# Kernel optimization log

Measured on AMD Instinct MI355X. Metric: run time of the kernel, lower is better.

The kernel has to match this reference:

```python
import jax, jax.numpy as jnp
import numpy as np

NH, D, MULT, NLAYER = 8, 512, 32, 3
N_INT = D * MULT // NH  # 2048 sparse-code dim per head
EPS = 1e-5
THETA = 2.0 ** 16
NUM_CLASSES = 2


def _ln(x):
    # LayerNorm over last dim, no affine (elementwise_affine=False), biased var
    m = jnp.mean(x, axis=-1, keepdims=True)
    v = jnp.mean((x - m) ** 2, axis=-1, keepdims=True)
    return (x - m) * jax.lax.rsqrt(v + EPS)


def _rotate_half(x):
    x1, x2 = jnp.split(x, 2, axis=-1)
    return jnp.concatenate((-x2, x1), axis=-1)


def _attn(Qs, V):
    # Qs: [B,nh,T,N] ReLU-sparse codes (Q == K), V: [B,1,T,D] raw hidden
    T = Qs.shape[2]
    half = 1.0 / (THETA ** (jnp.arange(0, N_INT, 2, dtype=jnp.float32) / N_INT))
    freqs = jnp.concatenate((half, half))                      # [N]
    ph = jnp.arange(T, dtype=jnp.float32)[:, None] * freqs[None, :]  # [T,N]
    QR = Qs * jnp.cos(ph) + _rotate_half(Qs) * jnp.sin(ph)
    scores = jnp.einsum('bhtn,bhsn->bhts', QR, QR)             # no softmax, no scaling
    mask = jnp.tril(jnp.ones((T, T), dtype=scores.dtype), k=-1)  # strictly causal
    scores = scores * mask
    return jnp.einsum('bhts,bsd->bhtd', scores, V[:, 0])       # [B,nh,T,D]


def setup_inputs():
    key = jax.random.key(0)
    ks = jax.random.split(key, 8)
    B, T, NA, F = 2, 1024, 93, 4
    in_dim, out_dim = NA * F, NA * NUM_CLASSES
    s = 0.02
    return dict(
        x=jax.random.normal(ks[0], (B, T, NA, F), dtype=jnp.float32),
        Wi=jax.random.normal(ks[1], (in_dim, D), dtype=jnp.float32) * s,
        bi=jnp.zeros((D,), jnp.float32),
        enc=jax.random.uniform(ks[2], (NH, D, N_INT), jnp.float32, -s, s),
        enc_v=jax.random.uniform(ks[3], (NH, D, N_INT), jnp.float32, -s, s),
        dec=jax.random.uniform(ks[4], (NH * N_INT, D), jnp.float32, -s, s),
        Wo=jax.random.normal(ks[5], (D, out_dim), dtype=jnp.float32) * s,
        bo=jnp.zeros((out_dim,), jnp.float32),
    )


def reference(x, Wi, bi, enc, enc_v, dec, Wo, bo):
    B, T, NA, F = x.shape
    h = _ln((x.reshape(B, T, NA * F) @ Wi + bi)[:, None])      # [B,1,T,D]
    for _ in range(NLAYER):
        h_res = h
        h_sp = jax.nn.relu(jnp.einsum('bxtd,hdn->bhtn', h, enc))      # [B,nh,T,N]
        yKV = _ln(_attn(h_sp, h))                                     # [B,nh,T,D]
        y_sp = jax.nn.relu(jnp.einsum('bhtd,hdn->bhtn', yKV, enc_v))  # [B,nh,T,N]
        xy = h_sp * y_sp                                              # gating
        # transpose(1,2).reshape(B,1,T,nh*N): head-major flatten of codes
        xy_flat = xy.transpose(0, 2, 1, 3).reshape(B, 1, T, NH * N_INT)
        h = _ln(h_res + _ln(xy_flat @ dec))                           # [B,1,T,D]
    out = h[:, 0] @ Wo + bo                                           # [B,T,NA*C]
    return out.reshape(B, T, NA, NUM_CLASSES)
```

## Files before the change

### kernel.cpp

```cpp
#include <hip/hip_runtime.h>

typedef __bf16 bf16;
typedef __attribute__((ext_vector_type(8))) __bf16 bf16x8;
typedef __attribute__((ext_vector_type(4))) float f32x4;
typedef __attribute__((ext_vector_type(2))) _Float16 h16x2;

#define T_SEQ 1024
#define D_MODEL 512
#define N_INT 2048
#define NHEADS 8
#define IN_DIM 372
#define IN_PAD 384
#define OUT_DIM 186
#define OUT_PAD 256

__device__ inline void gld16(const bf16* g, bf16* l) {
  __builtin_amdgcn_global_load_lds((const __attribute__((address_space(1))) void*)g,
                                   (__attribute__((address_space(3))) void*)l, 16, 0, 0);
}

__device__ inline void block_sum2(float& a, float& b, float* red) {
#pragma unroll
  for (int o = 32; o > 0; o >>= 1) {
    a += __shfl_down(a, o, 64);
    b += __shfl_down(b, o, 64);
  }
  __syncthreads();
  if ((threadIdx.x & 63) == 0) {
    int w = threadIdx.x >> 6;
    red[2 * w] = a;
    red[2 * w + 1] = b;
  }
  __syncthreads();
  a = red[0] + red[2] + red[4] + red[6];
  b = red[1] + red[3] + red[5] + red[7];
}

__global__ __launch_bounds__(256) void transpose_cvt(const float* __restrict__ in,
                                                     bf16* __restrict__ out,
                                                     int rows, int cols) {
  __shared__ float tile[32][33];
  size_t zoff = (size_t)blockIdx.z * rows * cols;
  in += zoff;
  out += zoff;
  int c0 = blockIdx.x * 32, r0 = blockIdx.y * 32;
#pragma unroll
  for (int i = threadIdx.y; i < 32; i += 8)
    tile[i][threadIdx.x] = in[(size_t)(r0 + i) * cols + c0 + threadIdx.x];
  __syncthreads();
#pragma unroll
  for (int i = threadIdx.y; i < 32; i += 8)
    out[(size_t)(c0 + i) * rows + r0 + threadIdx.x] = (bf16)tile[threadIdx.x][i];
}

__global__ __launch_bounds__(256) void pad_trans(const float* __restrict__ in,
                                                 bf16* __restrict__ out,
                                                 int R, int C, int outLd) {
  __shared__ float tile[32][33];
  int c0 = blockIdx.x * 32, r0 = blockIdx.y * 32;
#pragma unroll
  for (int i = threadIdx.y; i < 32; i += 8) {
    int r = r0 + i, c = c0 + threadIdx.x;
    tile[i][threadIdx.x] = (r < R && c < C) ? in[(size_t)r * C + c] : 0.f;
  }
  __syncthreads();
#pragma unroll
  for (int i = threadIdx.y; i < 32; i += 8)
    out[(size_t)(c0 + i) * outLd + r0 + threadIdx.x] = (bf16)tile[threadIdx.x][i];
}

__global__ __launch_bounds__(256) void cvt_pad_x(const float* __restrict__ x,
                                                 bf16* __restrict__ xbf) {
  size_t r = blockIdx.x;
  for (int c = threadIdx.x; c < IN_PAD; c += 256)
    xbf[r * IN_PAD + c] = (c < IN_DIM) ? (bf16)x[r * IN_DIM + c] : (bf16)0.f;
}

__global__ __launch_bounds__(256) void rope_tables(h16x2* __restrict__ cs) {
  int t = blockIdx.x;
  for (int i = threadIdx.x; i < 1024; i += 256) {
    float ph = (float)t * exp2f(-16.0f * (float)i * (1.0f / 1024.0f));
    h16x2 v;
    v[0] = (_Float16)cosf(ph);
    v[1] = (_Float16)sinf(ph);
    cs[(size_t)t * 1024 + i] = v;
  }
}

__global__ __launch_bounds__(256) void ln0(const float* __restrict__ zin,
                                           float* __restrict__ h, bf16* __restrict__ hbf,
                                           bf16* __restrict__ hT) {
  __shared__ float red[8];
  size_t r = blockIdx.x;
  int tid = threadIdx.x;
  float v0 = zin[r * 512 + tid], v1 = zin[r * 512 + tid + 256];
  float s = v0 + v1, s2 = v0 * v0 + v1 * v1;
  block_sum2(s, s2, red);
  float mean = s * (1.f / 512.f);
  float var = s2 * (1.f / 512.f) - mean * mean;
  float rs = rsqrtf(var + 1e-5f);
  float o0 = (v0 - mean) * rs, o1 = (v1 - mean) * rs;
  h[r * 512 + tid] = o0;
  h[r * 512 + tid + 256] = o1;
  hbf[r * 512 + tid] = (bf16)o0;
  hbf[r * 512 + tid + 256] = (bf16)o1;
  int b = (int)(r >> 10), t = (int)(r & (T_SEQ - 1));
  hT[((size_t)b * 512 + tid) * T_SEQ + t] = (bf16)o0;
  hT[((size_t)b * 512 + tid + 256) * T_SEQ + t] = (bf16)o1;
}

__global__ __launch_bounds__(256) void ln_rows(bf16* __restrict__ io) {
  const int wid = threadIdx.x >> 6, lane = threadIdx.x & 63;
  size_t r = (size_t)blockIdx.x * 4 + wid;
  bf16* p = io + r * 512 + lane * 8;
  bf16x8 v = *(const bf16x8*)p;
  float f[8], s = 0.f, s2 = 0.f;
#pragma unroll
  for (int j = 0; j < 8; ++j) {
    f[j] = (float)v[j];
    s += f[j];
    s2 += f[j] * f[j];
  }
#pragma unroll
  for (int o = 32; o > 0; o >>= 1) {
    s += __shfl_xor(s, o, 64);
    s2 += __shfl_xor(s2, o, 64);
  }
  float mean = s * (1.f / 512.f);
  float var = s2 * (1.f / 512.f) - mean * mean;
  float rs = rsqrtf(var + 1e-5f);
  bf16x8 o;
#pragma unroll
  for (int j = 0; j < 8; ++j) o[j] = (bf16)((f[j] - mean) * rs);
  *(bf16x8*)p = o;
}

__global__ __launch_bounds__(256) void psum_lnd(const bf16* __restrict__ part,
                                                float* __restrict__ h, bf16* __restrict__ hbf,
                                                bf16* __restrict__ hT, int b) {
  __shared__ float red[8];
  int r = blockIdx.x;
  int tid = threadIdx.x;
  float z0 = 0.f, z1 = 0.f;
#pragma unroll
  for (int k = 0; k < 16; ++k) {
    z0 += (float)part[((size_t)k << 19) + (size_t)r * 512 + tid];
    z1 += (float)part[((size_t)k << 19) + (size_t)r * 512 + tid + 256];
  }
  float s = z0 + z1, s2 = z0 * z0 + z1 * z1;
  block_sum2(s, s2, red);
  float m1 = s * (1.f / 512.f);
  float v1_ = s2 * (1.f / 512.f) - m1 * m1;
  float rs1 = rsqrtf(v1_ + 1e-5f);
  size_t R = (size_t)b * T_SEQ + r;
  float a0 = (z0 - m1) * rs1 + h[R * 512 + tid];
  float a1 = (z1 - m1) * rs1 + h[R * 512 + tid + 256];
  s = a0 + a1;
  s2 = a0 * a0 + a1 * a1;
  block_sum2(s, s2, red);
  float m2 = s * (1.f / 512.f);
  float v2_ = s2 * (1.f / 512.f) - m2 * m2;
  float rs2 = rsqrtf(v2_ + 1e-5f);
  float o0 = (a0 - m2) * rs2, o1 = (a1 - m2) * rs2;
  h[R * 512 + tid] = o0;
  h[R * 512 + tid + 256] = o1;
  hbf[R * 512 + tid] = (bf16)o0;
  hbf[R * 512 + tid + 256] = (bf16)o1;
  hT[((size_t)b * 512 + tid) * T_SEQ + r] = (bf16)o0;
  hT[((size_t)b * 512 + tid + 256) * T_SEQ + r] = (bf16)o1;
}

template <int MODE, int TN>
__device__ __forceinline__ void gemm_body(const bf16* __restrict__ Abase,
                                          const bf16* __restrict__ Bbase,
                                          const bf16* __restrict__ aux,
                                          const float* __restrict__ fbias,
                                          float* __restrict__ fout,
                                          bf16* __restrict__ bout) {
  const int id = blockIdx.x;
  int bz = 0, r_, chunk = 0;
  if constexpr (MODE >= 5) {
    r_ = id;
  } else if constexpr (MODE == 4) {
    r_ = id & 31;
    chunk = id >> 5;
  } else {
    bz = id & 7;
    r_ = id >> 3;
  }
  int bi, bj;
  if constexpr (MODE == 1) {
    int l = r_;
    bi = (int)sqrtf((float)l);
    while ((bi + 1) * (bi + 2) <= l) ++bi;
    while (bi * (bi + 1) > l) --bi;
    bj = l - bi * (bi + 1);
  } else if constexpr (MODE >= 5) {
    bi = r_ & 15;
    bj = r_ >> 4;
  } else {
    bi = r_ & 7;
    bj = r_ >> 3;
  }

  const bf16* A;
  const bf16* Bt;
  int lda, ldb, kend;
  if constexpr (MODE == 1) {
    A = Abase + (size_t)bz * T_SEQ * N_INT; lda = N_INT;
    Bt = A; ldb = N_INT;
    kend = N_INT;
  } else if constexpr (MODE == 2) {
    A = Abase + (size_t)bz * T_SEQ * T_SEQ; lda = T_SEQ;
    Bt = Bbase; ldb = T_SEQ;
    kend = (bi + 1) * 128;
  } else if constexpr (MODE == 3) {
    A = Abase + (size_t)bz * T_SEQ * 512; lda = 512;
    Bt = Bbase + (size_t)bz * N_INT * 512; ldb = 512;
    kend = 512;
  } else if constexpr (MODE == 4) {
    A = Abase + (size_t)chunk * 1024; lda = 16384;
    Bt = Bbase + (size_t)chunk * 1024; ldb = 16384;
    kend = 1024;
  } else if constexpr (MODE == 5) {
    A = Abase; lda = IN_PAD;
    Bt = Bbase; ldb = IN_PAD;
    kend = IN_PAD;
  } else {
    A = Abase; lda = 512;
    Bt = Bbase; ldb = 512;
    kend = 512;
  }

  const int tid = threadIdx.x;
  const int trow = tid >> 3, tq = tid & 7;
  const int sq = tq ^ (trow & 7);
  const bf16* ags = A + (size_t)(bi * 128 + trow) * lda + sq * 8;
  const bf16* bgs = Bt + (size_t)(bj * TN + trow) * ldb + sq * 8;

  __shared__ __align__(16) bf16 As[2][128 * 64];
  __shared__ __align__(16) bf16 Bs[2][TN * 64];
  const int so = tid * 8;

  const int lane = tid & 63, wid = tid >> 6;
  const int wr = wid >> 1, wc = wid & 1;
  const int fr = lane & 15, fg = lane >> 4;
  const int axor = fr & 7;
  constexpr int NR = TN / 32;

  f32x4 acc[4][NR] = {};

  auto stage = [&](int buf, int kk) {
#pragma unroll
    for (int p = 0; p < 4; ++p)
      gld16(ags + (size_t)(p * 32) * lda + kk, &As[buf][p * 2048 + so]);
#pragma unroll
    for (int p = 0; p < TN / 32; ++p)
      gld16(bgs + (size_t)(p * 32) * ldb + kk, &Bs[buf][p * 2048 + so]);
  };

  const int nt = kend >> 6;
  stage(0, 0);
  asm volatile("s_waitcnt vmcnt(0)" ::: "memory");
  __builtin_amdgcn_s_barrier();

  for (int t = 0; t < nt; ++t) {
    const int cur = t & 1;
    if (t + 1 < nt) stage(cur ^ 1, (t + 1) << 6);

    __builtin_amdgcn_s_setprio(1);
#pragma unroll
    for (int s = 0; s < 2; ++s) {
      bf16x8 af[4], bfv[NR];
#pragma unroll
      for (int m = 0; m < 4; ++m)
        af[m] = *(const bf16x8*)(&As[cur][(wr * 64 + m * 16 + fr) * 64 + (((s * 4 + fg) ^ axor) * 8)]);
#pragma unroll
      for (int n = 0; n < NR; ++n)
        bfv[n] = *(const bf16x8*)(&Bs[cur][(wc * (TN / 2) + n * 16 + fr) * 64 + (((s * 4 + fg) ^ axor) * 8)]);
#pragma unroll
      for (int m = 0; m < 4; ++m)
#pragma unroll
        for (int n = 0; n < NR; ++n)
          acc[m][n] = __builtin_amdgcn_mfma_f32_16x16x32_bf16(af[m], bfv[n], acc[m][n], 0, 0, 0);
    }
    __builtin_amdgcn_s_setprio(0);

    asm volatile("s_waitcnt vmcnt(0)" ::: "memory");
    __builtin_amdgcn_sched_barrier(0);
    __builtin_amdgcn_s_barrier();
    __builtin_amdgcn_sched_barrier(0);
  }

  if constexpr (MODE >= 5) {
#pragma unroll
    for (int m = 0; m < 4; ++m) {
#pragma unroll
      for (int n = 0; n < NR; ++n) {
        int c = bj * TN + wc * (TN / 2) + n * 16 + fr;
#pragma unroll
        for (int j = 0; j < 4; ++j) {
          int r = bi * 128 + wr * 64 + m * 16 + fg * 4 + j;
          float v = acc[m][n][j];
          if constexpr (MODE == 5) {
            fout[(size_t)r * 512 + c] = v + fbias[c];
          } else {
            if (c < OUT_DIM) fout[(size_t)r * OUT_DIM + c] = v + fbias[c];
          }
        }
      }
    }
  } else {
    bf16* stg = &As[0][0];
#pragma unroll
    for (int m = 0; m < 4; ++m)
#pragma unroll
      for (int n = 0; n < NR; ++n) {
        int lc = wc * (TN / 2) + n * 16 + fr;
#pragma unroll
        for (int j = 0; j < 4; ++j) {
          int lr = wr * 64 + m * 16 + fg * 4 + j;
          float v = acc[m][n][j];
          if constexpr (MODE == 3) v = fmaxf(v, 0.f);
          stg[lr * TN + lc] = (bf16)v;
        }
      }
    __syncthreads();
    constexpr int TPR = TN / 8;
    constexpr int RSTEP = 256 / TPR;
    const int c8 = (tid % TPR) * 8;
    const int lr0 = tid / TPR;
#pragma unroll
    for (int lr = lr0; lr < 128; lr += RSTEP) {
      bf16x8 v = *(const bf16x8*)&stg[lr * TN + c8];
      int r = bi * 128 + lr;
      int c = bj * TN + c8;
      if constexpr (MODE == 1) {
        bf16x8 o;
#pragma unroll
        for (int k = 0; k < 8; ++k) o[k] = (c + k < r) ? v[k] : (bf16)0.f;
        *(bf16x8*)&bout[(size_t)bz * T_SEQ * T_SEQ + (size_t)r * T_SEQ + c] = o;
      } else if constexpr (MODE == 2) {
        *(bf16x8*)&bout[((size_t)bz * T_SEQ + r) * 512 + c] = v;
      } else if constexpr (MODE == 3) {
        bf16x8 g = *(const bf16x8*)&aux[((size_t)bz * T_SEQ + r) * N_INT + c];
        bf16x8 o;
#pragma unroll
        for (int k = 0; k < 8; ++k) o[k] = (bf16)((float)v[k] * (float)g[k]);
        *(bf16x8*)&bout[(size_t)r * 16384 + (size_t)bz * N_INT + c] = o;
      } else {
        *(bf16x8*)&bout[((size_t)chunk << 19) + (size_t)r * 512 + c] = v;
      }
    }
  }
}

__global__ __launch_bounds__(256, 3) void g_scores(const bf16* A, bf16* o) {
  gemm_body<1, 64>(A, nullptr, nullptr, nullptr, nullptr, o);
}
__global__ __launch_bounds__(256, 3) void g_pv(const bf16* A, const bf16* B, bf16* o) {
  gemm_body<2, 64>(A, B, nullptr, nullptr, nullptr, o);
}
__global__ __launch_bounds__(256, 2) void g_gate(const bf16* A, const bf16* B, const bf16* aux, bf16* o) {
  gemm_body<3, 128>(A, B, aux, nullptr, nullptr, o);
}
__global__ __launch_bounds__(256, 2) void g_dec(const bf16* A, const bf16* B, bf16* o) {
  gemm_body<4, 128>(A, B, nullptr, nullptr, nullptr, o);
}
__global__ __launch_bounds__(256, 2) void g_in(const bf16* A, const bf16* B, const float* bias, float* o) {
  gemm_body<5, 128>(A, B, nullptr, bias, o, nullptr);
}
__global__ __launch_bounds__(256, 2) void g_out(const bf16* A, const bf16* B, const float* bias, float* o) {
  gemm_body<6, 128>(A, B, nullptr, bias, o, nullptr);
}

__global__ __launch_bounds__(256, 2) void g_hspr(const bf16* __restrict__ hbf_b,
                                                 const bf16* __restrict__ encT,
                                                 const h16x2* __restrict__ cs,
                                                 bf16* __restrict__ hsp,
                                                 bf16* __restrict__ qr) {
  const int id = blockIdx.x;
  const int bz = id & 7;
  const int r_ = id >> 3;
  const int bi = r_ & 7;
  const int bj = r_ >> 3;

  const bf16* B0 = encT + (size_t)bz * N_INT * 512 + (size_t)(bj * 64) * 512;
  const bf16* B1 = B0 + (size_t)1024 * 512;

  const int tid = threadIdx.x;
  const int trow = tid >> 3, tq = tid & 7;
  const int sq = tq ^ (trow & 7);
  const bf16* ags = hbf_b + (size_t)(bi * 128 + trow) * 512 + sq * 8;
  const bf16* bgs0 = B0 + (size_t)trow * 512 + sq * 8;
  const bf16* bgs1 = B1 + (size_t)trow * 512 + sq * 8;

  __shared__ __align__(16) bf16 As[2][128 * 64];
  __shared__ __align__(16) bf16 Bs[2][2 * 64 * 64];
  const int so = tid * 8;

  const int lane = tid & 63, wid = tid >> 6;
  const int wr = wid >> 1, wc = wid & 1;
  const int fr = lane & 15, fg = lane >> 4;
  const int axor = fr & 7;

  f32x4 acc[4][2][2] = {};

  auto stage = [&](int buf, int kk) {
#pragma unroll
    for (int p = 0; p < 4; ++p)
      gld16(ags + (size_t)(p * 32) * 512 + kk, &As[buf][p * 2048 + so]);
    gld16(bgs0 + kk, &Bs[buf][0 * 2048 + so]);
    gld16(bgs0 + (size_t)32 * 512 + kk, &Bs[buf][1 * 2048 + so]);
    gld16(bgs1 + kk, &Bs[buf][2 * 2048 + so]);
    gld16(bgs1 + (size_t)32 * 512 + kk, &Bs[buf][3 * 2048 + so]);
  };

  stage(0, 0);
  asm volatile("s_waitcnt vmcnt(0)" ::: "memory");
  __builtin_amdgcn_s_barrier();

  for (int t = 0; t < 8; ++t) {
    const int cur = t & 1;
    if (t + 1 < 8) stage(cur ^ 1, (t + 1) << 6);

    __builtin_amdgcn_s_setprio(1);
#pragma unroll
    for (int s = 0; s < 2; ++s) {
      bf16x8 af[4], bfv[2][2];
#pragma unroll
      for (int m = 0; m < 4; ++m)
        af[m] = *(const bf16x8*)(&As[cur][(wr * 64 + m * 16 + fr) * 64 + (((s * 4 + fg) ^ axor) * 8)]);
#pragma unroll
      for (int pp = 0; pp < 2; ++pp)
#pragma unroll
        for (int n = 0; n < 2; ++n)
          bfv[pp][n] = *(const bf16x8*)(&Bs[cur][pp * 4096 + (wc * 32 + n * 16 + fr) * 64 + (((s * 4 + fg) ^ axor) * 8)]);
#pragma unroll
      for (int m = 0; m < 4; ++m)
#pragma unroll
        for (int n = 0; n < 2; ++n)
#pragma unroll
          for (int pp = 0; pp < 2; ++pp)
            acc[m][n][pp] = __builtin_amdgcn_mfma_f32_16x16x32_bf16(af[m], bfv[pp][n], acc[m][n][pp], 0, 0, 0);
    }
    __builtin_amdgcn_s_setprio(0);

    asm volatile("s_waitcnt vmcnt(0)" ::: "memory");
    __builtin_amdgcn_sched_barrier(0);
    __builtin_amdgcn_s_barrier();
    __builtin_amdgcn_sched_barrier(0);
  }

  bf16* sL = &As[0][0];
  bf16* sH = &As[1][0];
#pragma unroll
  for (int m = 0; m < 4; ++m)
#pragma unroll
    for (int n = 0; n < 2; ++n) {
      int lc = wc * 32 + n * 16 + fr;
#pragma unroll
      for (int j = 0; j < 4; ++j) {
        int lr = wr * 64 + m * 16 + fg * 4 + j;
        sL[lr * 64 + lc] = (bf16)fmaxf(acc[m][n][0][j], 0.f);
        sH[lr * 64 + lc] = (bf16)fmaxf(acc[m][n][1][j], 0.f);
      }
    }
  __syncthreads();

  const size_t hb = (size_t)bz * T_SEQ;
  const int c8 = (tid & 7) * 8;
  const int lr0 = tid >> 3;
#pragma unroll
  for (int lr = lr0; lr < 128; lr += 32) {
    int r = bi * 128 + lr;
    int c = bj * 64 + c8;
    bf16x8 lo = *(const bf16x8*)&sL[lr * 64 + c8];
    bf16x8 hi = *(const bf16x8*)&sH[lr * 64 + c8];
    size_t base = (hb + r) * N_INT + c;
    *(bf16x8*)&hsp[base] = lo;
    *(bf16x8*)&hsp[base + 1024] = hi;
    const h16x2* csp = &cs[(size_t)r * 1024 + c];
    bf16x8 qlo, qhi;
#pragma unroll
    for (int k = 0; k < 8; ++k) {
      h16x2 p = csp[k];
      float co = (float)p[0], si = (float)p[1];
      float v0 = (float)lo[k], v1 = (float)hi[k];
      qlo[k] = (bf16)(v0 * co - v1 * si);
      qhi[k] = (bf16)(v1 * co + v0 * si);
    }
    *(bf16x8*)&qr[base] = qlo;
    *(bf16x8*)&qr[base + 1024] = qhi;
  }
}

extern "C" void kernel_launch(void* const* d_in, const int* in_sizes, int n_in,
                              void* d_out, int out_size, void* d_ws, size_t ws_size,
                              hipStream_t stream) {
  const float* x = (const float*)d_in[0];
  const float* Wi = (const float*)d_in[1];
  const float* bi = (const float*)d_in[2];
  const float* enc = (const float*)d_in[3];
  const float* encv = (const float*)d_in[4];
  const float* dec = (const float*)d_in[5];
  const float* Wo = (const float*)d_in[6];
  const float* bo = (const float*)d_in[7];
  float* out = (float*)d_out;

  const size_t NEED = 163840000;
  if (ws_size < NEED) return;

  char* w = (char*)d_ws;
  auto alloc = [&](size_t bytes) {
    char* p = w;
    w += (bytes + 255) & ~(size_t)255;
    return p;
  };
  bf16* encT = (bf16*)alloc((size_t)NHEADS * N_INT * 512 * 2);
  bf16* encvT = (bf16*)alloc((size_t)NHEADS * N_INT * 512 * 2);
  bf16* decT = (bf16*)alloc((size_t)512 * 16384 * 2);
  h16x2* cs = (h16x2*)alloc((size_t)T_SEQ * 1024 * 4);
  float* h = (float*)alloc((size_t)2048 * 512 * 4);
  bf16* hbf = (bf16*)alloc((size_t)2048 * 512 * 2);
  bf16* hT = (bf16*)alloc((size_t)2048 * 512 * 2);
  bf16* hsp = (bf16*)alloc((size_t)NHEADS * T_SEQ * N_INT * 2);
  bf16* qr = (bf16*)alloc((size_t)NHEADS * T_SEQ * N_INT * 2);
  bf16* S = (bf16*)alloc((size_t)NHEADS * T_SEQ * T_SEQ * 2);
  bf16* ykv = (bf16*)alloc((size_t)NHEADS * T_SEQ * 512 * 2);
  float* zbuf = (float*)alloc((size_t)2048 * 512 * 4);
  bf16* WoT = (bf16*)alloc((size_t)OUT_PAD * 512 * 2);
  bf16* xbf = S;
  bf16* WiT = S + 1048576;

  transpose_cvt<<<dim3(64, 16, 8), dim3(32, 8), 0, stream>>>(enc, encT, 512, N_INT);
  transpose_cvt<<<dim3(64, 16, 8), dim3(32, 8), 0, stream>>>(encv, encvT, 512, N_INT);
  transpose_cvt<<<dim3(16, 512, 1), dim3(32, 8), 0, stream>>>(dec, decT, 16384, 512);
  pad_trans<<<dim3(16, 12), dim3(32, 8), 0, stream>>>(Wi, WiT, IN_DIM, 512, IN_PAD);
  pad_trans<<<dim3(8, 16), dim3(32, 8), 0, stream>>>(Wo, WoT, 512, OUT_DIM, 512);
  cvt_pad_x<<<2048, 256, 0, stream>>>(x, xbf);
  rope_tables<<<1024, 256, 0, stream>>>(cs);
  g_in<<<64, 256, 0, stream>>>(xbf, WiT, bi, zbuf);
  ln0<<<2048, 256, 0, stream>>>(zbuf, h, hbf, hT);

  for (int L = 0; L < 3; ++L) {
    for (int b = 0; b < 2; ++b) {
      const bf16* hbf_b = hbf + (size_t)b * T_SEQ * 512;
      const bf16* hT_b = hT + (size_t)b * 512 * T_SEQ;
      g_hspr<<<1024, 256, 0, stream>>>(hbf_b, encT, cs, hsp, qr);
      g_scores<<<576, 256, 0, stream>>>(qr, S);
      g_pv<<<512, 256, 0, stream>>>(S, hT_b, ykv);
      ln_rows<<<2048, 256, 0, stream>>>(ykv);
      g_gate<<<1024, 256, 0, stream>>>(ykv, encvT, hsp, qr);
      g_dec<<<512, 256, 0, stream>>>(qr, decT, S);
      psum_lnd<<<1024, 256, 0, stream>>>(S, h, hbf, hT, b);
    }
  }
  g_out<<<32, 256, 0, stream>>>(hbf, WoT, bo, out);
}
```

Measured before the change: 985.5 us.

## Batch both sequences into each layer launch to double grid sizes

Removes the per-batch loop and launches every layer kernel over both batch elements at once, folding the batch index into the block id and doubling the intermediate buffers (hsp, qr, S, ykv). The intent is to halve the kernel launch count and give each grid twice as many blocks, so the GPU stays better occupied, especially in the smaller grids such as g_scores and g_pv. The cost is roughly double the workspace footprint, a larger required workspace size, and more pressure on cache/HBM from the bigger working set.

```diff
diff --git a/kernel.cpp b/kernel.cpp
--- a/kernel.cpp
+++ b/kernel.cpp
@@ -137,15 +137,17 @@
 
 __global__ __launch_bounds__(256) void psum_lnd(const bf16* __restrict__ part,
                                                 float* __restrict__ h, bf16* __restrict__ hbf,
-                                                bf16* __restrict__ hT, int b) {
+                                                bf16* __restrict__ hT) {
   __shared__ float red[8];
-  int r = blockIdx.x;
+  int b = blockIdx.x >> 10;
+  int r = blockIdx.x & 1023;
   int tid = threadIdx.x;
   float z0 = 0.f, z1 = 0.f;
 #pragma unroll
   for (int k = 0; k < 16; ++k) {
-    z0 += (float)part[((size_t)k << 19) + (size_t)r * 512 + tid];
-    z1 += (float)part[((size_t)k << 19) + (size_t)r * 512 + tid + 256];
+    size_t off = ((size_t)(b * 16 + k) << 19) + (size_t)r * 512;
+    z0 += (float)part[off + tid];
+    z1 += (float)part[off + tid + 256];
   }
   float s = z0 + z1, s2 = z0 * z0 + z1 * z1;
   block_sum2(s, s2, red);
@@ -178,15 +180,15 @@
                                           float* __restrict__ fout,
                                           bf16* __restrict__ bout) {
   const int id = blockIdx.x;
-  int bz = 0, r_, chunk = 0;
+  int zz = 0, r_, cb = 0;
   if constexpr (MODE >= 5) {
     r_ = id;
   } else if constexpr (MODE == 4) {
     r_ = id & 31;
-    chunk = id >> 5;
+    cb = id >> 5;
   } else {
-    bz = id & 7;
-    r_ = id >> 3;
+    zz = id & 15;
+    r_ = id >> 4;
   }
   int bi, bj;
   if constexpr (MODE == 1) {
@@ -207,20 +209,20 @@
   const bf16* Bt;
   int lda, ldb, kend;
   if constexpr (MODE == 1) {
-    A = Abase + (size_t)bz * T_SEQ * N_INT; lda = N_INT;
+    A = Abase + ((size_t)zz << 21); lda = N_INT;
     Bt = A; ldb = N_INT;
     kend = N_INT;
   } else if constexpr (MODE == 2) {
-    A = Abase + (size_t)bz * T_SEQ * T_SEQ; lda = T_SEQ;
-    Bt = Bbase; ldb = T_SEQ;
+    A = Abase + ((size_t)zz << 20); lda = T_SEQ;
+    Bt = Bbase + (size_t)(zz >> 3) * 512 * T_SEQ; ldb = T_SEQ;
     kend = (bi + 1) * 128;
   } else if constexpr (MODE == 3) {
-    A = Abase + (size_t)bz * T_SEQ * 512; lda = 512;
-    Bt = Bbase + (size_t)bz * N_INT * 512; ldb = 512;
+    A = Abase + ((size_t)zz << 19); lda = 512;
+    Bt = Bbase + (size_t)(zz & 7) * N_INT * 512; ldb = 512;
     kend = 512;
   } else if constexpr (MODE == 4) {
-    A = Abase + (size_t)chunk * 1024; lda = 16384;
-    Bt = Bbase + (size_t)chunk * 1024; ldb = 16384;
+    A = Abase + ((size_t)(cb >> 4) << 24) + (size_t)(cb & 15) * 1024; lda = 16384;
+    Bt = Bbase + (size_t)(cb & 15) * 1024; ldb = 16384;
     kend = 1024;
   } else if constexpr (MODE == 5) {
     A = Abase; lda = IN_PAD;
@@ -339,17 +341,17 @@
         bf16x8 o;
 #pragma unroll
         for (int k = 0; k < 8; ++k) o[k] = (c + k < r) ? v[k] : (bf16)0.f;
-        *(bf16x8*)&bout[(size_t)bz * T_SEQ * T_SEQ + (size_t)r * T_SEQ + c] = o;
+        *(bf16x8*)&bout[((size_t)zz << 20) + (size_t)r * T_SEQ + c] = o;
       } else if constexpr (MODE == 2) {
-        *(bf16x8*)&bout[((size_t)bz * T_SEQ + r) * 512 + c] = v;
+        *(bf16x8*)&bout[((size_t)zz << 19) + (size_t)r * 512 + c] = v;
       } else if constexpr (MODE == 3) {
-        bf16x8 g = *(const bf16x8*)&aux[((size_t)bz * T_SEQ + r) * N_INT + c];
+        bf16x8 g = *(const bf16x8*)&aux[((size_t)zz << 21) + (size_t)r * N_INT + c];
         bf16x8 o;
 #pragma unroll
         for (int k = 0; k < 8; ++k) o[k] = (bf16)((float)v[k] * (float)g[k]);
-        *(bf16x8*)&bout[(size_t)r * 16384 + (size_t)bz * N_INT + c] = o;
+        *(bf16x8*)&bout[((size_t)(zz >> 3) << 24) + (size_t)r * 16384 + (size_t)(zz & 7) * N_INT + c] = o;
       } else {
-        *(bf16x8*)&bout[((size_t)chunk << 19) + (size_t)r * 512 + c] = v;
+        *(bf16x8*)&bout[((size_t)cb << 19) + (size_t)r * 512 + c] = v;
       }
     }
   }
@@ -374,19 +376,20 @@
   gemm_body<6, 128>(A, B, nullptr, bias, o, nullptr);
 }
 
-__global__ __launch_bounds__(256, 2) void g_hspr(const bf16* __restrict__ hbf_b,
+__global__ __launch_bounds__(256, 2) void g_hspr(const bf16* __restrict__ hbf,
                                                  const bf16* __restrict__ encT,
                                                  const h16x2* __restrict__ cs,
                                                  bf16* __restrict__ hsp,
                                                  bf16* __restrict__ qr) {
   const int id = blockIdx.x;
-  const int bz = id & 7;
-  const int r_ = id >> 3;
+  const int zz = id & 15;
+  const int r_ = id >> 4;
   const int bi = r_ & 7;
   const int bj = r_ >> 3;
 
-  const bf16* B0 = encT + (size_t)bz * N_INT * 512 + (size_t)(bj * 64) * 512;
+  const bf16* B0 = encT + (size_t)(zz & 7) * N_INT * 512 + (size_t)(bj * 64) * 512;
   const bf16* B1 = B0 + (size_t)1024 * 512;
+  const bf16* hbf_b = hbf + (size_t)(zz >> 3) * T_SEQ * 512;
 
   const int tid = threadIdx.x;
   const int trow = tid >> 3, tq = tid & 7;
@@ -468,7 +471,7 @@
     }
   __syncthreads();
 
-  const size_t hb = (size_t)bz * T_SEQ;
+  const size_t hb = (size_t)zz * T_SEQ;
   const int c8 = (tid & 7) * 8;
   const int lr0 = tid >> 3;
 #pragma unroll
@@ -508,7 +511,7 @@
   const float* bo = (const float*)d_in[7];
   float* out = (float*)d_out;
 
-  const size_t NEED = 163840000;
+  const size_t NEED = 253000000;
   if (ws_size < NEED) return;
 
   char* w = (char*)d_ws;
@@ -524,10 +527,10 @@
   float* h = (float*)alloc((size_t)2048 * 512 * 4);
   bf16* hbf = (bf16*)alloc((size_t)2048 * 512 * 2);
   bf16* hT = (bf16*)alloc((size_t)2048 * 512 * 2);
-  bf16* hsp = (bf16*)alloc((size_t)NHEADS * T_SEQ * N_INT * 2);
-  bf16* qr = (bf16*)alloc((size_t)NHEADS * T_SEQ * N_INT * 2);
-  bf16* S = (bf16*)alloc((size_t)NHEADS * T_SEQ * T_SEQ * 2);
-  bf16* ykv = (bf16*)alloc((size_t)NHEADS * T_SEQ * 512 * 2);
+  bf16* hsp = (bf16*)alloc((size_t)2 * NHEADS * T_SEQ * N_INT * 2);
+  bf16* qr = (bf16*)alloc((size_t)2 * NHEADS * T_SEQ * N_INT * 2);
+  bf16* S = (bf16*)alloc((size_t)2 * NHEADS * T_SEQ * T_SEQ * 2);
+  bf16* ykv = (bf16*)alloc((size_t)2 * NHEADS * T_SEQ * 512 * 2);
   float* zbuf = (float*)alloc((size_t)2048 * 512 * 4);
   bf16* WoT = (bf16*)alloc((size_t)OUT_PAD * 512 * 2);
   bf16* xbf = S;
@@ -544,17 +547,13 @@
   ln0<<<2048, 256, 0, stream>>>(zbuf, h, hbf, hT);
 
   for (int L = 0; L < 3; ++L) {
-    for (int b = 0; b < 2; ++b) {
-      const bf16* hbf_b = hbf + (size_t)b * T_SEQ * 512;
-      const bf16* hT_b = hT + (size_t)b * 512 * T_SEQ;
-      g_hspr<<<1024, 256, 0, stream>>>(hbf_b, encT, cs, hsp, qr);
-      g_scores<<<576, 256, 0, stream>>>(qr, S);
-      g_pv<<<512, 256, 0, stream>>>(S, hT_b, ykv);
-      ln_rows<<<2048, 256, 0, stream>>>(ykv);
-      g_gate<<<1024, 256, 0, stream>>>(ykv, encvT, hsp, qr);
-      g_dec<<<512, 256, 0, stream>>>(qr, decT, S);
-      psum_lnd<<<1024, 256, 0, stream>>>(S, h, hbf, hT, b);
-    }
+    g_hspr<<<2048, 256, 0, stream>>>(hbf, encT, cs, hsp, qr);
+    g_scores<<<1152, 256, 0, stream>>>(qr, S);
+    g_pv<<<1024, 256, 0, stream>>>(S, hT, ykv);
+    ln_rows<<<4096, 256, 0, stream>>>(ykv);
+    g_gate<<<2048, 256, 0, stream>>>(ykv, encvT, hsp, qr);
+    g_dec<<<1024, 256, 0, stream>>>(qr, decT, S);
+    psum_lnd<<<2048, 256, 0, stream>>>(S, h, hbf, hT);
   }
   g_out<<<32, 256, 0, stream>>>(hbf, WoT, bo, out);
 }
```

Result: faster. 883.4 us (-10.4%).
